# Performance work log

Hardware: AMD Instinct MI355X
Metric: run time of the kernel (lower is better)

## Reference

```python
import jax, jax.numpy as jnp
import numpy as np

IN_C, OUT_C = 128, 256
KH, KW = 3, 3
STRIDE = (1, 1)
PAD = (1, 1)


def setup_inputs() -> dict:
    key = jax.random.key(0)
    kx, kw = jax.random.split(key)
    x = jax.random.normal(kx, (32, IN_C, 56, 56), dtype=jnp.float32)
    k = 1.0 / (IN_C * KH * KW)
    weight = (2.0 * jax.random.uniform(kw, (OUT_C, IN_C, KH, KW), dtype=jnp.float32) - 1.0) * (k ** 0.5)
    return {"x": x, "weight": weight}


def reference(x, weight):
    # Equivalent to the as_strided broadcast-multiply-sum: a plain 2D cross-correlation
    # (no bias), NCHW input, OIHW weight, stride (1,1), padding (1,1).
    return jax.lax.conv_general_dilated(
        x, weight,
        window_strides=STRIDE,
        padding=[(PAD[0], PAD[0]), (PAD[1], PAD[1])],
        dimension_numbers=("NCHW", "OIHW", "NCHW"),
    )
```

## Files before the change

kernel.cpp:

```cpp
#include <hip/hip_runtime.h>

typedef __attribute__((ext_vector_type(8))) short short8;
typedef __attribute__((ext_vector_type(4))) float floatx4;

#define IN_C 128
#define OUT_C 256
#define NB 32
#define HW 56
#define S_PER_N (HW * HW)
#define M_TOTAL (NB * S_PER_N)
#define PH 58
#define PW 66
#define XN_ELEMS (NB * PH * PW * IN_C)
#define WT_ELEMS (9 * OUT_C * IN_C)

__device__ __forceinline__ unsigned short f2bf(float f) {
    unsigned int u = __builtin_bit_cast(unsigned int, f);
    u = (u + 0x7FFFu + ((u >> 16) & 1u)) >> 16;
    return (unsigned short)u;
}

__device__ __forceinline__ void gld_lds16(const unsigned short* g, unsigned short* l) {
    __builtin_amdgcn_global_load_lds(
        (const __attribute__((address_space(1))) unsigned int*)g,
        (__attribute__((address_space(3))) unsigned int*)l, 16, 0, 0);
}

__global__ void xform_x(const float* __restrict__ x, unsigned short* __restrict__ xn) {
    const int ihp = blockIdx.x;
    const int n   = blockIdx.y;
    const int tid = threadIdx.x;
    unsigned int* __restrict__ row32 =
        (unsigned int*)(xn + (size_t)(n * PH + ihp) * PW * IN_C);
    const int WORDS = PW * IN_C / 2;

    if (ihp == 0 || ihp == PH - 1) {
        for (int i = tid; i < WORDS; i += 256) row32[i] = 0u;
        return;
    }
    const int ih = ihp - 1;
    __shared__ float lds[IN_C][HW + 1];
    const float* __restrict__ xrow = x + (size_t)n * IN_C * S_PER_N + (size_t)ih * HW;
    for (int i = tid; i < IN_C * 14; i += 256) {
        int ic = i / 14, iw4 = (i % 14) * 4;
        float4 v = *(const float4*)(xrow + (size_t)ic * S_PER_N + iw4);
        lds[ic][iw4 + 0] = v.x;
        lds[ic][iw4 + 1] = v.y;
        lds[ic][iw4 + 2] = v.z;
        lds[ic][iw4 + 3] = v.w;
    }
    __syncthreads();
    for (int wi = tid; wi < WORDS; wi += 256) {
        int pix = wi >> 6;
        int ic  = (wi & 63) * 2;
        unsigned int val = 0u;
        if (pix >= 1 && pix <= HW) {
            int iw = pix - 1;
            unsigned int lo = f2bf(lds[ic][iw]);
            unsigned int hi = f2bf(lds[ic + 1][iw]);
            val = (hi << 16) | lo;
        }
        row32[wi] = val;
    }
}

__global__ void xform_w(const float* __restrict__ w, unsigned short* __restrict__ wt) {
    const int idx = blockIdx.x * 256 + threadIdx.x;
    const int ic  = idx & 127;
    const int oc  = (idx >> 7) & 255;
    const int khw = idx >> 15;
    wt[idx] = f2bf(w[(oc * IN_C + ic) * 9 + khw]);
}

__global__ void __launch_bounds__(256)
conv_mfma(const unsigned short* __restrict__ xn,
          const unsigned short* __restrict__ wt,
          float* __restrict__ out) {
    const int tid  = threadIdx.x;
    const int lane = tid & 63;
    const int wv   = tid >> 6;
    const int l15  = lane & 15;
    const int quad = lane >> 4;

    const int bx      = blockIdx.x;
    const int tile_oc = bx & 1;
    const int tile_m  = bx >> 1;

    const int s_blk  = tile_m * 128;
    const int oc_blk = tile_oc * 128;
    const int s0  = s_blk + (wv & 1) * 64;
    const int oc0 = oc_blk + (wv >> 1) * 64;

    __shared__ unsigned short A_lds[128 * 32];
    __shared__ unsigned short B_lds[128 * 32];

    const int srow = tid >> 2;
    const int sic  = (tid & 3) * 8;

    const unsigned short* a_g0 = wt + (size_t)(oc_blk + srow) * IN_C + sic;
    const unsigned short* a_g1 = a_g0 + 64 * IN_C;

    const unsigned short* b_g[2];
#pragma unroll
    for (int q = 0; q < 2; ++q) {
        int sg = s_blk + q * 64 + srow;
        int n  = sg / S_PER_N;
        int r  = sg % S_PER_N;
        int oh = r / HW, ow = r % HW;
        b_g[q] = xn + (size_t)((n * PH + oh) * PW + ow) * IN_C + sic;
    }
    unsigned short* a_l0 = A_lds + tid * 8;
    unsigned short* a_l1 = A_lds + 2048 + tid * 8;
    unsigned short* b_l0 = B_lds + tid * 8;
    unsigned short* b_l1 = B_lds + 2048 + tid * 8;

    int afo[4], bfo[4];
#pragma unroll
    for (int i = 0; i < 4; ++i)
        afo[i] = ((wv >> 1) * 64 + i * 16 + l15) * 32 + quad * 8;
#pragma unroll
    for (int j = 0; j < 4; ++j)
        bfo[j] = ((wv & 1) * 64 + j * 16 + l15) * 32 + quad * 8;

    floatx4 acc[4][4];
#pragma unroll
    for (int i = 0; i < 4; ++i)
#pragma unroll
        for (int j = 0; j < 4; ++j) acc[i][j] = (floatx4){0.f, 0.f, 0.f, 0.f};

#pragma unroll
    for (int khw = 0; khw < 9; ++khw) {
        const int xo = ((khw / 3) * PW + (khw % 3)) * IN_C;
        const int wo = khw * OUT_C * IN_C;
#pragma unroll
        for (int st = 0; st < 4; ++st) {
            const int ic0 = st * 32;
            __syncthreads();
            gld_lds16(a_g0 + wo + ic0, a_l0);
            gld_lds16(a_g1 + wo + ic0, a_l1);
            gld_lds16(b_g[0] + xo + ic0, b_l0);
            gld_lds16(b_g[1] + xo + ic0, b_l1);
            __syncthreads();

            short8 a[4], b[4];
#pragma unroll
            for (int i = 0; i < 4; ++i) a[i] = *(const short8*)(A_lds + afo[i]);
#pragma unroll
            for (int j = 0; j < 4; ++j) b[j] = *(const short8*)(B_lds + bfo[j]);
#pragma unroll
            for (int i = 0; i < 4; ++i)
#pragma unroll
                for (int j = 0; j < 4; ++j)
                    acc[i][j] = __builtin_amdgcn_mfma_f32_16x16x32_bf16(
                        a[i], b[j], acc[i][j], 0, 0, 0);
        }
    }

#pragma unroll
    for (int j = 0; j < 4; ++j) {
        int s_glob = s0 + j * 16 + l15;
        int n = s_glob / S_PER_N;
        int s = s_glob % S_PER_N;
        float* obase = out + (size_t)n * OUT_C * S_PER_N + s;
#pragma unroll
        for (int i = 0; i < 4; ++i) {
            int oc = oc0 + i * 16 + quad * 4;
#pragma unroll
            for (int r = 0; r < 4; ++r)
                obase[(size_t)(oc + r) * S_PER_N] = acc[i][j][r];
        }
    }
}

extern "C" void kernel_launch(void* const* d_in, const int* in_sizes, int n_in,
                              void* d_out, int out_size, void* d_ws, size_t ws_size,
                              hipStream_t stream) {
    const float* x = (const float*)d_in[0];
    const float* w = (const float*)d_in[1];
    float* out = (float*)d_out;

    unsigned short* xn = (unsigned short*)d_ws;
    unsigned short* wt = xn + XN_ELEMS;

    dim3 gx(PH, NB);
    xform_x<<<gx, 256, 0, stream>>>(x, xn);
    xform_w<<<WT_ELEMS / 256, 256, 0, stream>>>(w, wt);
    conv_mfma<<<(M_TOTAL / 128) * 2, 256, 0, stream>>>(xn, wt, out);
}
```

Measured before the change: 223.3 us.

## Double K-tile depth to 64 per sync and convert to bf16 before LDS transpose

The conv kernel now stages 64 input channels per barrier pair instead of 32, halving the number of __syncthreads and load rounds per output tile. LDS grows to 32 KB per block, and a launch bound of 3 blocks per CU is added. The x-transform kernel converts to bf16 during the load into a pixel-major LDS layout, so the write-out reads packed words directly. The wider LDS rows (128 bytes) may cause bank conflicts on fragment reads, and the larger footprint may reduce occupancy.

Result: faster. 217.4 us (-2.6%).

```diff
diff --git a/kernel.cpp b/kernel.cpp
--- a/kernel.cpp
+++ b/kernel.cpp
@@ -39,27 +39,23 @@
         return;
     }
     const int ih = ihp - 1;
-    __shared__ float lds[IN_C][HW + 1];
+    __shared__ unsigned short lds2[HW][IN_C];
     const float* __restrict__ xrow = x + (size_t)n * IN_C * S_PER_N + (size_t)ih * HW;
     for (int i = tid; i < IN_C * 14; i += 256) {
         int ic = i / 14, iw4 = (i % 14) * 4;
         float4 v = *(const float4*)(xrow + (size_t)ic * S_PER_N + iw4);
-        lds[ic][iw4 + 0] = v.x;
-        lds[ic][iw4 + 1] = v.y;
-        lds[ic][iw4 + 2] = v.z;
-        lds[ic][iw4 + 3] = v.w;
+        lds2[iw4 + 0][ic] = f2bf(v.x);
+        lds2[iw4 + 1][ic] = f2bf(v.y);
+        lds2[iw4 + 2][ic] = f2bf(v.z);
+        lds2[iw4 + 3][ic] = f2bf(v.w);
     }
     __syncthreads();
     for (int wi = tid; wi < WORDS; wi += 256) {
         int pix = wi >> 6;
-        int ic  = (wi & 63) * 2;
+        int icw = wi & 63;
         unsigned int val = 0u;
-        if (pix >= 1 && pix <= HW) {
-            int iw = pix - 1;
-            unsigned int lo = f2bf(lds[ic][iw]);
-            unsigned int hi = f2bf(lds[ic + 1][iw]);
-            val = (hi << 16) | lo;
-        }
+        if (pix >= 1 && pix <= HW)
+            val = *(const unsigned int*)&lds2[pix - 1][icw * 2];
         row32[wi] = val;
     }
 }
@@ -72,7 +68,7 @@
     wt[idx] = f2bf(w[(oc * IN_C + ic) * 9 + khw]);
 }
 
-__global__ void __launch_bounds__(256)
+__global__ void __launch_bounds__(256, 3)
 conv_mfma(const unsigned short* __restrict__ xn,
           const unsigned short* __restrict__ wt,
           float* __restrict__ out) {
@@ -91,36 +87,34 @@
     const int s0  = s_blk + (wv & 1) * 64;
     const int oc0 = oc_blk + (wv >> 1) * 64;
 
-    __shared__ unsigned short A_lds[128 * 32];
-    __shared__ unsigned short B_lds[128 * 32];
+    __shared__ unsigned short A_lds[128 * 64];
+    __shared__ unsigned short B_lds[128 * 64];
 
-    const int srow = tid >> 2;
-    const int sic  = (tid & 3) * 8;
+    const int srow = tid >> 3;
+    const int sic  = (tid & 7) * 8;
 
-    const unsigned short* a_g0 = wt + (size_t)(oc_blk + srow) * IN_C + sic;
-    const unsigned short* a_g1 = a_g0 + 64 * IN_C;
-
-    const unsigned short* b_g[2];
+    const unsigned short* a_g[4];
+    const unsigned short* b_g[4];
 #pragma unroll
-    for (int q = 0; q < 2; ++q) {
-        int sg = s_blk + q * 64 + srow;
+    for (int q = 0; q < 4; ++q) {
+        int row = q * 32 + srow;
+        a_g[q] = wt + (size_t)(oc_blk + row) * IN_C + sic;
+        int sg = s_blk + row;
         int n  = sg / S_PER_N;
         int r  = sg % S_PER_N;
         int oh = r / HW, ow = r % HW;
         b_g[q] = xn + (size_t)((n * PH + oh) * PW + ow) * IN_C + sic;
     }
-    unsigned short* a_l0 = A_lds + tid * 8;
-    unsigned short* a_l1 = A_lds + 2048 + tid * 8;
-    unsigned short* b_l0 = B_lds + tid * 8;
-    unsigned short* b_l1 = B_lds + 2048 + tid * 8;
+    unsigned short* a_l = A_lds + tid * 8;
+    unsigned short* b_l = B_lds + tid * 8;
 
     int afo[4], bfo[4];
 #pragma unroll
     for (int i = 0; i < 4; ++i)
-        afo[i] = ((wv >> 1) * 64 + i * 16 + l15) * 32 + quad * 8;
+        afo[i] = ((wv >> 1) * 64 + i * 16 + l15) * 64 + quad * 8;
 #pragma unroll
     for (int j = 0; j < 4; ++j)
-        bfo[j] = ((wv & 1) * 64 + j * 16 + l15) * 32 + quad * 8;
+        bfo[j] = ((wv & 1) * 64 + j * 16 + l15) * 64 + quad * 8;
 
     floatx4 acc[4][4];
 #pragma unroll
@@ -133,26 +127,31 @@
         const int xo = ((khw / 3) * PW + (khw % 3)) * IN_C;
         const int wo = khw * OUT_C * IN_C;
 #pragma unroll
-        for (int st = 0; st < 4; ++st) {
-            const int ic0 = st * 32;
+        for (int h = 0; h < 2; ++h) {
+            const int ic0 = h * 64;
             __syncthreads();
-            gld_lds16(a_g0 + wo + ic0, a_l0);
-            gld_lds16(a_g1 + wo + ic0, a_l1);
-            gld_lds16(b_g[0] + xo + ic0, b_l0);
-            gld_lds16(b_g[1] + xo + ic0, b_l1);
+#pragma unroll
+            for (int q = 0; q < 4; ++q) {
+                gld_lds16(a_g[q] + wo + ic0, a_l + q * 2048);
+                gld_lds16(b_g[q] + xo + ic0, b_l + q * 2048);
+            }
             __syncthreads();
 
-            short8 a[4], b[4];
 #pragma unroll
-            for (int i = 0; i < 4; ++i) a[i] = *(const short8*)(A_lds + afo[i]);
+            for (int kk = 0; kk < 2; ++kk) {
+                const int ko = kk * 32;
+                short8 a[4], b[4];
 #pragma unroll
-            for (int j = 0; j < 4; ++j) b[j] = *(const short8*)(B_lds + bfo[j]);
+                for (int i = 0; i < 4; ++i) a[i] = *(const short8*)(A_lds + afo[i] + ko);
 #pragma unroll
-            for (int i = 0; i < 4; ++i)
+                for (int j = 0; j < 4; ++j) b[j] = *(const short8*)(B_lds + bfo[j] + ko);
 #pragma unroll
-                for (int j = 0; j < 4; ++j)
-                    acc[i][j] = __builtin_amdgcn_mfma_f32_16x16x32_bf16(
-                        a[i], b[j], acc[i][j], 0, 0, 0);
+                for (int i = 0; i < 4; ++i)
+#pragma unroll
+                    for (int j = 0; j < 4; ++j)
+                        acc[i][j] = __builtin_amdgcn_mfma_f32_16x16x32_bf16(
+                            a[i], b[j], acc[i][j], 0, 0, 0);
+            }
         }
     }
 
```
